# Kernel optimization log

Hardware: AMD Instinct MI355X
Metric: run time of the kernel (lower is better)

The kernel has to match this reference:

```python
import jax, jax.numpy as jnp
import numpy as np

N, E = 50000, 800000
IN_C, OUT_C, HEADS = 128, 16, 8
EDGE_DIM = 1
NEG_SLOPE = 0.2
LN_EPS = 1e-5


def setup_inputs() -> dict:
    key = jax.random.key(0)
    ks = jax.random.split(key, 12)
    s = 1.0 / np.sqrt(IN_C)
    HC = OUT_C * HEADS
    return {
        "x": jax.random.normal(ks[0], (N, IN_C), jnp.float32),
        "edge_index": jax.random.randint(ks[1], (2, E), 0, N, jnp.int32),
        "edge_attr": jax.random.normal(ks[2], (E, EDGE_DIM), jnp.float32),
        "W": jax.random.normal(ks[3], (IN_C, HC), jnp.float32) * s,
        "b": jnp.zeros((HC,), jnp.float32),
        "att_src": jax.random.normal(ks[4], (HEADS, OUT_C), jnp.float32) * s,
        "att_dst": jax.random.normal(ks[5], (HEADS, OUT_C), jnp.float32) * s,
        "att_edge": jax.random.normal(ks[6], (HEADS, OUT_C), jnp.float32) * s,
        "lin_edge_w": jax.random.normal(ks[7], (EDGE_DIM, HC), jnp.float32) * s,
        "lin_edge_b": jnp.zeros((HC,), jnp.float32),
        "gamma": jnp.ones((HC,), jnp.float32),
        "beta": jnp.zeros((HC,), jnp.float32),
    }


def _segment_softmax(logits, seg, num_segments):
    # numerically-stable softmax over edges grouped by destination node
    m = jax.ops.segment_max(logits, seg, num_segments=num_segments)
    ex = jnp.exp(logits - m[seg])
    z = jax.ops.segment_sum(ex, seg, num_segments=num_segments)
    return ex / (z[seg] + 1e-16)


def reference(x, edge_index, edge_attr, W, b, att_src, att_dst, att_edge,
              lin_edge_w, lin_edge_b, gamma, beta):
    n = x.shape[0]
    src, dst = edge_index[0], edge_index[1]
    # GAT conv: per-head transform, edge-indexed attention, segment softmax, scatter-add
    h = (x @ W).reshape(n, HEADS, OUT_C)                      # [N,H,C]
    a_src = jnp.einsum('nhc,hc->nh', h, att_src)              # [N,H]
    a_dst = jnp.einsum('nhc,hc->nh', h, att_dst)
    e = (edge_attr @ lin_edge_w + lin_edge_b).reshape(-1, HEADS, OUT_C)
    a_edge = jnp.einsum('ehc,hc->eh', e, att_edge)            # [E,H]
    logits = jax.nn.leaky_relu(a_src[src] + a_dst[dst] + a_edge, NEG_SLOPE)
    alpha = _segment_softmax(logits, dst, n)                  # [E,H]
    msg = alpha[..., None] * h[src]                           # [E,H,C]
    out = jax.ops.segment_sum(msg, dst, num_segments=n).reshape(n, -1) + b
    # residual (in_channels == heads*out_channels -> identity projection)
    out = out + x
    # LayerNorm + ELU (dropout is eval-mode identity)
    mu = jnp.mean(out, axis=-1, keepdims=True)
    var = jnp.var(out, axis=-1, keepdims=True)
    out = (out - mu) * jax.lax.rsqrt(var + LN_EPS) * gamma + beta
    return jax.nn.elu(out)
```

## Files before the change

kernel.cpp:

```cpp
#include <hip/hip_runtime.h>
#include <hip/hip_bf16.h>

#define N_NODES 50000
#define N_EDGES 800000
#define IN_C 128
#define HC 128
#define HEADS 8
#define NEG_SLOPE 0.2f
#define LN_EPS 1e-5f

#define LDH 136
#define ELL_CAP 64
#define GEMM_BLOCKS 782
#define FILL_BLOCKS 782
#define FUSED_BLOCKS (GEMM_BLOCKS + FILL_BLOCKS)
#define NBUCK 98
#define BCAP 26
#define OVF_CAP 4096

typedef __hip_bfloat16 bf16;
typedef __attribute__((ext_vector_type(8))) short short8;
typedef __attribute__((ext_vector_type(4))) float f32x4;
typedef unsigned long long u64;

__device__ __forceinline__ float b2f(bf16 v) { return __bfloat162float(v); }

__device__ __forceinline__ unsigned short f2bf(float f) {
    unsigned u = __float_as_uint(f);
    return (unsigned short)((u + 0x7fffu + ((u >> 16) & 1u)) >> 16);
}
__device__ __forceinline__ float bf2f(unsigned s) {
    return __uint_as_float(s << 16);
}
__device__ __forceinline__ short8 pack8(float4 u, float4 v) {
    short8 r;
    r[0] = (short)f2bf(u.x); r[1] = (short)f2bf(u.y);
    r[2] = (short)f2bf(u.z); r[3] = (short)f2bf(u.w);
    r[4] = (short)f2bf(v.x); r[5] = (short)f2bf(v.y);
    r[6] = (short)f2bf(v.z); r[7] = (short)f2bf(v.w);
    return r;
}

union FusedSm {
    short sH[4][16 * LDH];
    struct {
        u64 recs[NBUCK][BCAP];
        int lcnt[NBUCK];
    } bin;
};

__global__ __launch_bounds__(256) void prep(
    const float* __restrict__ W, unsigned short* __restrict__ Wt,
    int* __restrict__ ovfc)
{
    int id = blockIdx.x * 256 + threadIdx.x;
    int k = id >> 7, n = id & 127;
    Wt[n * 128 + k] = f2bf(W[id]);
    if (id == 0) *ovfc = 0;
}

__device__ __forceinline__ void gemm_body(
    int gid, int t,
    const float* __restrict__ x, const unsigned short* __restrict__ Wt,
    const float* __restrict__ att_src, const float* __restrict__ att_dst,
    unsigned short* __restrict__ h_out,
    float* __restrict__ a_src, float* __restrict__ a_dst,
    short (*sH)[16 * LDH])
{
    const int wv  = t >> 6;
    const int l   = t & 63;
    const int gw  = gid * 4 + wv;
    if (gw >= N_NODES / 16) return;

    const int n0   = gw * 16;
    const int mrow = l & 15;
    const int quad = l >> 4;

    short8 afrag[4];
    const float* xr = x + (size_t)(n0 + mrow) * IN_C + quad * 8;
#pragma unroll
    for (int ko = 0; ko < 4; ++ko) {
        float4 u = *reinterpret_cast<const float4*>(xr + ko * 32);
        float4 v = *reinterpret_cast<const float4*>(xr + ko * 32 + 4);
        afrag[ko] = pack8(u, v);
    }

    f32x4 acc[8];
#pragma unroll
    for (int nt = 0; nt < 8; ++nt) acc[nt] = (f32x4)0.f;
#pragma unroll
    for (int nt = 0; nt < 8; ++nt) {
        const unsigned short* wr = Wt + (nt * 16 + mrow) * 128 + quad * 8;
#pragma unroll
        for (int ko = 0; ko < 4; ++ko) {
            short8 bfr = *reinterpret_cast<const short8*>(wr + ko * 32);
            acc[nt] = __builtin_amdgcn_mfma_f32_16x16x32_bf16(afrag[ko], bfr, acc[nt], 0, 0, 0);
        }
    }

#pragma unroll
    for (int nt = 0; nt < 8; ++nt)
#pragma unroll
        for (int r = 0; r < 4; ++r)
            sH[wv][(quad * 4 + r) * LDH + nt * 16 + mrow] = (short)f2bf(acc[nt][r]);

#pragma unroll
    for (int i = 0; i < 4; ++i) {
        int row = i * 4 + (l >> 4);
        int col = (l & 15) * 8;
        short8 hv = *reinterpret_cast<const short8*>(&sH[wv][row * LDH + col]);
        *reinterpret_cast<short8*>(h_out + (size_t)(n0 + row) * HC + col) = hv;
    }

#pragma unroll
    for (int pp = 0; pp < 2; ++pp) {
        int p  = l + pp * 64;
        int m  = p >> 3;
        int hd = p & 7;
        float ssum = 0.f, dsum = 0.f;
#pragma unroll
        for (int c = 0; c < 16; ++c) {
            float hv = bf2f((unsigned short)sH[wv][m * LDH + hd * 16 + c]);
            ssum = fmaf(hv, att_src[hd * 16 + c], ssum);
            dsum = fmaf(hv, att_dst[hd * 16 + c], dsum);
        }
        a_src[(n0 + m) * HEADS + hd] = ssum;
        a_dst[(n0 + m) * HEADS + hd] = dsum;
    }
}

__global__ __launch_bounds__(256) void fused(
    const float* __restrict__ x, const unsigned short* __restrict__ Wt,
    const float* __restrict__ att_src, const float* __restrict__ att_dst,
    const int* __restrict__ ei, const float* __restrict__ edge_attr,
    u64* __restrict__ arena, unsigned short* __restrict__ bcnt,
    int* __restrict__ ovfc, u64* __restrict__ ovf,
    unsigned short* __restrict__ h_out,
    float* __restrict__ a_src, float* __restrict__ a_dst)
{
    __shared__ FusedSm sm;
    const int bid = blockIdx.x;
    const int t   = threadIdx.x;

    if (bid & 1) {
        const int blk = bid >> 1;
        if (t < NBUCK) sm.bin.lcnt[t] = 0;
        __syncthreads();

        const int e0 = blk * 1024 + t * 4;
        if (e0 < N_EDGES) {
            const int4   s4 = *reinterpret_cast<const int4*>(ei + e0);
            const int4   d4 = *reinterpret_cast<const int4*>(ei + N_EDGES + e0);
            const float4 a4 = *reinterpret_cast<const float4*>(edge_attr + e0);
#define BIN1(D, S, A)                                                      \
            {                                                              \
                const unsigned w_ =                                        \
                    (((unsigned)(S)) << 16) | (unsigned)f2bf(A);           \
                const int b_ = (D) >> 9;                                   \
                int p_ = atomicAdd(&sm.bin.lcnt[b_], 1);                   \
                if (p_ < BCAP)                                             \
                    sm.bin.recs[b_][p_] =                                  \
                        ((u64)(unsigned)((D) & 511) << 32) | (u64)w_;      \
                else {                                                     \
                    int op_ = atomicAdd(ovfc, 1);                          \
                    if (op_ < OVF_CAP)                                     \
                        ovf[op_] = ((u64)(unsigned)(D) << 32) | (u64)w_;   \
                }                                                          \
            }
            BIN1(d4.x, s4.x, a4.x)
            BIN1(d4.y, s4.y, a4.y)
            BIN1(d4.z, s4.z, a4.z)
            BIN1(d4.w, s4.w, a4.w)
#undef BIN1
        }
        __syncthreads();
        if (t < NBUCK) {
            int k = min(sm.bin.lcnt[t], BCAP);
            sm.bin.lcnt[t] = k;
            bcnt[blk * NBUCK + t] = (unsigned short)k;
        }
        __syncthreads();
        for (int i = t; i < NBUCK * BCAP; i += 256) {
            const int bi = i / BCAP;
            const int j  = i - bi * BCAP;
            if (j < sm.bin.lcnt[bi])
                arena[((size_t)bi * FILL_BLOCKS + blk) * BCAP + j] =
                    sm.bin.recs[bi][j];
        }
        return;
    }

    gemm_body(bid >> 1, t, x, Wt, att_src, att_dst, h_out, a_src, a_dst, sm.sH);
}

__global__ __launch_bounds__(1024) void ebuild(
    const u64* __restrict__ arena, const unsigned short* __restrict__ bcnt,
    const int* __restrict__ ovfc, const u64* __restrict__ ovf,
    unsigned int* __restrict__ ellp, int* __restrict__ cnt)
{
    __shared__ int lc[512];
    __shared__ unsigned short sbc[FILL_BLOCKS];
    const int t = threadIdx.x;
    const int b = blockIdx.x;
    if (t < 512) lc[t] = 0;
    if (t < FILL_BLOCKS) sbc[t] = bcnt[t * NBUCK + b];
    __syncthreads();

    const u64* seg = arena + (size_t)b * (FILL_BLOCKS * BCAP);
    for (int q = t; q < FILL_BLOCKS * BCAP; q += 1024) {
        const int blk = q / BCAP;
        const int sl  = q - blk * BCAP;
        if (sl < (int)sbc[blk]) {
            const u64 rec = seg[q];
            const int dl = (int)(rec >> 32);
            int p = atomicAdd(&lc[dl], 1);
            if (p < ELL_CAP)
                ellp[((size_t)((b << 9) + dl) << 6) + p] = (unsigned)rec;
        }
    }
    const int ovn = min(*ovfc, OVF_CAP);
    for (int q = t; q < ovn; q += 1024) {
        const u64 rec = ovf[q];
        const int n = (int)(rec >> 32);
        if ((n >> 9) == b) {
            int p = atomicAdd(&lc[n & 511], 1);
            if (p < ELL_CAP)
                ellp[((size_t)n << 6) + p] = (unsigned)rec;
        }
    }
    __syncthreads();
    if (t < 512) {
        const int n = (b << 9) + t;
        if (n < N_NODES) cnt[n] = min(lc[t], ELL_CAP);
    }
}


#define LROW(CE, HV, J, OFF, B0)                                           \
    { int cj_ = __builtin_amdgcn_ds_swizzle((int)(CE), OFF);               \
      size_t r_ = ((B0) + (J) < cn) ? (size_t)(((unsigned)cj_) >> 16) : 0; \
      (HV)[J] = h2[r_ * 64 + l]; }
#define LOADROWS(CE, HV, B0)                                               \
    LROW(CE, HV, 0,  24, B0) LROW(CE, HV, 1,  56, B0)                      \
    LROW(CE, HV, 2,  88, B0) LROW(CE, HV, 3, 120, B0)                      \
    LROW(CE, HV, 4, 152, B0) LROW(CE, HV, 5, 184, B0)                      \
    LROW(CE, HV, 6, 216, B0) LROW(CE, HV, 7, 248, B0)

#define FROW(EV, HV, J, OFF)                                               \
    { float evj_ = __uint_as_float((unsigned)__builtin_amdgcn_ds_swizzle(  \
          __float_as_int(EV), OFF));                                       \
      acc0 = fmaf(evj_, b2f((HV)[J].x), acc0);                             \
      acc1 = fmaf(evj_, b2f((HV)[J].y), acc1); }
#define FMAROWS(EV, HV)                                                    \
    FROW(EV, HV, 0,  24) FROW(EV, HV, 1,  56) FROW(EV, HV, 2,  88)        \
    FROW(EV, HV, 3, 120) FROW(EV, HV, 4, 152) FROW(EV, HV, 5, 184)        \
    FROW(EV, HV, 6, 216) FROW(EV, HV, 7, 248)

__global__ __launch_bounds__(256) void gather_node(
    const int* __restrict__ cnt, const unsigned int* __restrict__ ellp,
    const float* __restrict__ a_src, const float* __restrict__ a_dst,
    const bf16* __restrict__ h,
    const float* __restrict__ x, const float* __restrict__ bvec,
    const float* __restrict__ gamma, const float* __restrict__ beta,
    const float* __restrict__ att_edge, const float* __restrict__ lin_w,
    const float* __restrict__ lin_b,
    float* __restrict__ out)
{
    const int wave = threadIdx.x >> 6;
    const int l    = threadIdx.x & 63;
    const int n    = blockIdx.x * 4 + wave;
    const int hh   = l >> 3;
    const int jj   = l & 7;

    float ae0 = att_edge[2 * l], ae1 = att_edge[2 * l + 1];
    float p = ae0 * lin_w[2 * l] + ae1 * lin_w[2 * l + 1];
    float q = ae0 * lin_b[2 * l] + ae1 * lin_b[2 * l + 1];
#pragma unroll
    for (int off = 1; off <= 4; off <<= 1) {
        p += __shfl_xor(p, off, 64);
        q += __shfl_xor(q, off, 64);
    }
    const float2 bv = *reinterpret_cast<const float2*>(bvec + 2 * l);
    const float2 gv = *reinterpret_cast<const float2*>(gamma + 2 * l);
    const float2 be = *reinterpret_cast<const float2*>(beta + 2 * l);

    const float adq = a_dst[n * HEADS + hh] + q;
    const int   beg = n << 6;
    const int   cn  = min(cnt[n], ELL_CAP);

    float zp = 0.f, acc0 = 0.f, acc1 = 0.f;
    const __hip_bfloat162* h2 = reinterpret_cast<const __hip_bfloat162*>(h);

    if (cn > 0) {
        unsigned ce_c = ellp[beg + jj];
        float    as_c = a_src[(ce_c >> 16) * HEADS + hh];
        __hip_bfloat162 hv_c[8], hv_n[8];
        LOADROWS(ce_c, hv_c, 0)

        for (int bs = 0; ; bs += 8) {
            const unsigned ce   = ce_c;
            const float    as   = as_c;
            const bool     last = (bs + 8 >= cn);
            if (!last) {
                ce_c = ellp[beg + bs + 8 + jj];
                LOADROWS(ce_c, hv_n, bs + 8)
                as_c = a_src[(ce_c >> 16) * HEADS + hh];
            }
            const float ea = bf2f(ce & 0xffffu);
            float lg = fmaf(ea, p, as + adq);
            lg = fmaxf(lg, NEG_SLOPE * lg);
            const float ev = (bs + jj < cn) ? __expf(lg) : 0.f;
            zp += ev;
            FMAROWS(ev, hv_c)
            if (last) break;
#pragma unroll
            for (int j = 0; j < 8; ++j) hv_c[j] = hv_n[j];
        }
    }

    float z = zp;
    z += __shfl_xor(z, 1, 64);
    z += __shfl_xor(z, 2, 64);
    z += __shfl_xor(z, 4, 64);
    const float rz = 1.f / (z + 1e-16f);
    acc0 *= rz;
    acc1 *= rz;

    const size_t idx = (size_t)n * HC + 2 * l;
    const float2 xv = *reinterpret_cast<const float2*>(x + idx);
    float v0 = acc0 + xv.x + bv.x;
    float v1 = acc1 + xv.y + bv.y;
    float s1 = v0 + v1, s2 = v0 * v0 + v1 * v1;
#pragma unroll
    for (int off = 32; off >= 1; off >>= 1) {
        s1 += __shfl_xor(s1, off, 64);
        s2 += __shfl_xor(s2, off, 64);
    }
    const float mean = s1 * (1.f / HC);
    const float var  = s2 * (1.f / HC) - mean * mean;
    const float inv  = rsqrtf(var + LN_EPS);
    float y0 = (v0 - mean) * inv * gv.x + be.x;
    float y1 = (v1 - mean) * inv * gv.y + be.y;
    y0 = y0 > 0.f ? y0 : expm1f(y0);
    y1 = y1 > 0.f ? y1 : expm1f(y1);
    *reinterpret_cast<float2*>(out + idx) = make_float2(y0, y1);
}

extern "C" void kernel_launch(void* const* d_in, const int* in_sizes, int n_in,
                              void* d_out, int out_size, void* d_ws, size_t ws_size,
                              hipStream_t stream)
{
    const float* x         = (const float*)d_in[0];
    const int*   ei        = (const int*)d_in[1];
    const float* edge_attr = (const float*)d_in[2];
    const float* W         = (const float*)d_in[3];
    const float* b         = (const float*)d_in[4];
    const float* att_src   = (const float*)d_in[5];
    const float* att_dst   = (const float*)d_in[6];
    const float* att_edge  = (const float*)d_in[7];
    const float* lin_w     = (const float*)d_in[8];
    const float* lin_b     = (const float*)d_in[9];
    const float* gamma     = (const float*)d_in[10];
    const float* beta      = (const float*)d_in[11];

    char* ws = (char*)d_ws;
    bf16*  h     = (bf16*)ws;  ws += (size_t)N_NODES * HC * sizeof(bf16);
    float* a_src = (float*)ws; ws += (size_t)N_NODES * HEADS * sizeof(float);
    float* a_dst = (float*)ws; ws += (size_t)N_NODES * HEADS * sizeof(float);
    int*   cnt   = (int*)ws;   ws += (size_t)N_NODES * sizeof(int);
    unsigned short* Wt = (unsigned short*)ws;
    ws += (size_t)128 * 128 * sizeof(unsigned short);
    unsigned int* ellp = (unsigned int*)ws;
    ws += (size_t)(N_NODES * ELL_CAP + 64) * sizeof(unsigned int);
    unsigned short* bcnt = (unsigned short*)ws;
    ws += (size_t)FILL_BLOCKS * NBUCK * sizeof(unsigned short);
    int* ovfc = (int*)ws;      ws += 64;
    u64* ovf  = (u64*)ws;      ws += (size_t)OVF_CAP * sizeof(u64);
    u64* arena = (u64*)d_out;

    prep<<<64, 256, 0, stream>>>(W, Wt, ovfc);

    fused<<<FUSED_BLOCKS, 256, 0, stream>>>(
        x, Wt, att_src, att_dst, ei, edge_attr, arena, bcnt, ovfc, ovf,
        (unsigned short*)h, a_src, a_dst);

    ebuild<<<NBUCK, 1024, 0, stream>>>(arena, bcnt, ovfc, ovf, ellp, cnt);

    gather_node<<<N_NODES / 4, 256, 0, stream>>>(
        cnt, ellp, a_src, a_dst, h, x, b, gamma, beta,
        att_edge, lin_w, lin_b, (float*)d_out);
}
```

Baseline: 191.5 us.

## Use finer 128-node buckets and sentinel-padded arena slots in edge binning

The edge binning step now uses 392 buckets of 128 destination nodes with 8 slots per block-bucket instead of 98 buckets of 512 nodes with 26 slots. Unused slots are filled with a sentinel, which removes the per-block bucket-count array and its extra barrier. The ELL build kernel runs 392 blocks of 256 threads that skip sentinel records rather than 98 blocks of 1024 threads. This spreads the build work over more CUs and shrinks shared-memory counters. In exchange every slot is always written, and the smaller per-bucket capacity sends more edges to the global overflow list, which every build block must scan.

```diff
diff --git a/kernel.cpp b/kernel.cpp
--- a/kernel.cpp
+++ b/kernel.cpp
@@ -14,9 +14,10 @@
 #define GEMM_BLOCKS 782
 #define FILL_BLOCKS 782
 #define FUSED_BLOCKS (GEMM_BLOCKS + FILL_BLOCKS)
-#define NBUCK 98
-#define BCAP 26
-#define OVF_CAP 4096
+#define NBUCK 392
+#define BCAP 8
+#define OVF_CAP 8192
+#define SENT 0xFFFFFFFFFFFFFFFFull
 
 typedef __hip_bfloat16 bf16;
 typedef __attribute__((ext_vector_type(8))) short short8;
@@ -133,8 +134,7 @@
     const float* __restrict__ x, const unsigned short* __restrict__ Wt,
     const float* __restrict__ att_src, const float* __restrict__ att_dst,
     const int* __restrict__ ei, const float* __restrict__ edge_attr,
-    u64* __restrict__ arena, unsigned short* __restrict__ bcnt,
-    int* __restrict__ ovfc, u64* __restrict__ ovf,
+    u64* __restrict__ arena, int* __restrict__ ovfc, u64* __restrict__ ovf,
     unsigned short* __restrict__ h_out,
     float* __restrict__ a_src, float* __restrict__ a_dst)
 {
@@ -144,7 +144,7 @@
 
     if (bid & 1) {
         const int blk = bid >> 1;
-        if (t < NBUCK) sm.bin.lcnt[t] = 0;
+        for (int i = t; i < NBUCK; i += 256) sm.bin.lcnt[i] = 0;
         __syncthreads();
 
         const int e0 = blk * 1024 + t * 4;
@@ -156,11 +156,11 @@
             {                                                              \
                 const unsigned w_ =                                        \
                     (((unsigned)(S)) << 16) | (unsigned)f2bf(A);           \
-                const int b_ = (D) >> 9;                                   \
+                const int b_ = (D) >> 7;                                   \
                 int p_ = atomicAdd(&sm.bin.lcnt[b_], 1);                   \
                 if (p_ < BCAP)                                             \
                     sm.bin.recs[b_][p_] =                                  \
-                        ((u64)(unsigned)((D) & 511) << 32) | (u64)w_;      \
+                        ((u64)(unsigned)((D) & 127) << 32) | (u64)w_;      \
                 else {                                                     \
                     int op_ = atomicAdd(ovfc, 1);                          \
                     if (op_ < OVF_CAP)                                     \
@@ -174,18 +174,11 @@
 #undef BIN1
         }
         __syncthreads();
-        if (t < NBUCK) {
-            int k = min(sm.bin.lcnt[t], BCAP);
-            sm.bin.lcnt[t] = k;
-            bcnt[blk * NBUCK + t] = (unsigned short)k;
-        }
-        __syncthreads();
         for (int i = t; i < NBUCK * BCAP; i += 256) {
-            const int bi = i / BCAP;
-            const int j  = i - bi * BCAP;
-            if (j < sm.bin.lcnt[bi])
-                arena[((size_t)bi * FILL_BLOCKS + blk) * BCAP + j] =
-                    sm.bin.recs[bi][j];
+            const int bi = i >> 3;
+            const int j  = i & 7;
+            u64 v = (j < sm.bin.lcnt[bi]) ? sm.bin.recs[bi][j] : SENT;
+            arena[((size_t)bi * FILL_BLOCKS + blk) * BCAP + j] = v;
         }
         return;
     }
@@ -193,44 +186,40 @@
     gemm_body(bid >> 1, t, x, Wt, att_src, att_dst, h_out, a_src, a_dst, sm.sH);
 }
 
-__global__ __launch_bounds__(1024) void ebuild(
-    const u64* __restrict__ arena, const unsigned short* __restrict__ bcnt,
-    const int* __restrict__ ovfc, const u64* __restrict__ ovf,
+__global__ __launch_bounds__(256) void ebuild(
+    const u64* __restrict__ arena, const int* __restrict__ ovfc,
+    const u64* __restrict__ ovf,
     unsigned int* __restrict__ ellp, int* __restrict__ cnt)
 {
-    __shared__ int lc[512];
-    __shared__ unsigned short sbc[FILL_BLOCKS];
+    __shared__ int lc[128];
     const int t = threadIdx.x;
     const int b = blockIdx.x;
-    if (t < 512) lc[t] = 0;
-    if (t < FILL_BLOCKS) sbc[t] = bcnt[t * NBUCK + b];
+    if (t < 128) lc[t] = 0;
     __syncthreads();
 
     const u64* seg = arena + (size_t)b * (FILL_BLOCKS * BCAP);
-    for (int q = t; q < FILL_BLOCKS * BCAP; q += 1024) {
-        const int blk = q / BCAP;
-        const int sl  = q - blk * BCAP;
-        if (sl < (int)sbc[blk]) {
-            const u64 rec = seg[q];
+    for (int q = t; q < FILL_BLOCKS * BCAP; q += 256) {
+        const u64 rec = seg[q];
+        if (rec != SENT) {
             const int dl = (int)(rec >> 32);
             int p = atomicAdd(&lc[dl], 1);
             if (p < ELL_CAP)
-                ellp[((size_t)((b << 9) + dl) << 6) + p] = (unsigned)rec;
+                ellp[((size_t)((b << 7) + dl) << 6) + p] = (unsigned)rec;
         }
     }
     const int ovn = min(*ovfc, OVF_CAP);
-    for (int q = t; q < ovn; q += 1024) {
+    for (int q = t; q < ovn; q += 256) {
         const u64 rec = ovf[q];
         const int n = (int)(rec >> 32);
-        if ((n >> 9) == b) {
-            int p = atomicAdd(&lc[n & 511], 1);
+        if ((n >> 7) == b) {
+            int p = atomicAdd(&lc[n & 127], 1);
             if (p < ELL_CAP)
                 ellp[((size_t)n << 6) + p] = (unsigned)rec;
         }
     }
     __syncthreads();
-    if (t < 512) {
-        const int n = (b << 9) + t;
+    if (t < 128) {
+        const int n = (b << 7) + t;
         if (n < N_NODES) cnt[n] = min(lc[t], ELL_CAP);
     }
 }
@@ -372,8 +361,6 @@
     ws += (size_t)128 * 128 * sizeof(unsigned short);
     unsigned int* ellp = (unsigned int*)ws;
     ws += (size_t)(N_NODES * ELL_CAP + 64) * sizeof(unsigned int);
-    unsigned short* bcnt = (unsigned short*)ws;
-    ws += (size_t)FILL_BLOCKS * NBUCK * sizeof(unsigned short);
     int* ovfc = (int*)ws;      ws += 64;
     u64* ovf  = (u64*)ws;      ws += (size_t)OVF_CAP * sizeof(u64);
     u64* arena = (u64*)d_out;
@@ -381,10 +368,10 @@
     prep<<<64, 256, 0, stream>>>(W, Wt, ovfc);
 
     fused<<<FUSED_BLOCKS, 256, 0, stream>>>(
-        x, Wt, att_src, att_dst, ei, edge_attr, arena, bcnt, ovfc, ovf,
+        x, Wt, att_src, att_dst, ei, edge_attr, arena, ovfc, ovf,
         (unsigned short*)h, a_src, a_dst);
 
-    ebuild<<<NBUCK, 1024, 0, stream>>>(arena, bcnt, ovfc, ovf, ellp, cnt);
+    ebuild<<<NBUCK, 256, 0, stream>>>(arena, ovfc, ovf, ellp, cnt);
 
     gather_node<<<N_NODES / 4, 256, 0, stream>>>(
         cnt, ellp, a_src, a_dst, h, x, b, gamma, beta,
```

Measured after the change: 191.4 us. No clear change (-0.1%).
